# Optimization experiments

Measured on AMD Instinct MI355X. Metric: run time of the kernel, lower is better.

Reference implementation:

```python
import jax, jax.numpy as jnp
import numpy as np

B, IN, HID, EMB, K = 65536, 256, 256, 64, 4096
EPS = 1e-5  # BatchNorm1d default eps


def setup_inputs() -> dict:
    key = jax.random.key(0)
    ks = jax.random.split(key, 12)
    s = 0.05
    return {
        "x": jax.random.normal(ks[0], (B, IN), jnp.float32),
        "W1": jax.random.normal(ks[1], (HID, IN), jnp.float32) * s,
        "b1": jax.random.normal(ks[2], (HID,), jnp.float32) * s,
        "gamma": jnp.ones((HID,), jnp.float32),
        "beta": jnp.zeros((HID,), jnp.float32),
        "mean": jax.random.normal(ks[3], (HID,), jnp.float32) * s,
        "var": jax.random.uniform(ks[4], (HID,), jnp.float32, 0.5, 1.5),
        "W2": jax.random.normal(ks[5], (HID // 2, HID), jnp.float32) * s,
        "b2": jax.random.normal(ks[6], (HID // 2,), jnp.float32) * s,
        "W3": jax.random.normal(ks[7], (EMB, HID // 2), jnp.float32) * s,
        "b3": jax.random.normal(ks[8], (EMB,), jnp.float32) * s,
        "codebook": jax.random.normal(ks[9], (K, EMB), jnp.float32),
    }


def reference(x, W1, b1, gamma, beta, mean, var, W2, b2, W3, b3, codebook):
    # encoder: Linear -> BatchNorm1d (eval stats) -> ReLU -> Linear -> ReLU -> Linear -> Tanh
    h = x @ W1.T + b1                                   # [B, HID]
    h = (h - mean) * jax.lax.rsqrt(var + EPS) * gamma + beta
    h = jax.nn.relu(h)
    h = jax.nn.relu(h @ W2.T + b2)                      # [B, HID//2]
    z = jnp.tanh(h @ W3.T + b3)                         # [B, EMB]
    # squared-distance matrix: ||z||^2 + ||e||^2 - 2 z e^T  -> [B, K]
    d = (jnp.sum(z * z, axis=1, keepdims=True)
         + jnp.sum(codebook * codebook, axis=1)
         - 2.0 * (z @ codebook.T))
    return jnp.argmin(d, axis=1)                        # [B] int token indices
```

## Files before the change

### kernel.cpp

```cpp
#include <hip/hip_runtime.h>

#define IN_DIM  256
#define HID_DIM 256
#define H2_DIM  128
#define EMB_DIM 64
#define K_CODES 4096
#define EPS_BN  1e-5f


typedef _Float16 f16;
typedef _Float16 f16x4 __attribute__((ext_vector_type(4)));
typedef _Float16 f16x8 __attribute__((ext_vector_type(8)));
typedef float    f32x16 __attribute__((ext_vector_type(16)));

__global__ __launch_bounds__(256) void k_norms(const float* __restrict__ cb,
                                               float* __restrict__ norms) {
    int c = blockIdx.x * 256 + threadIdx.x;
    const float4* row = reinterpret_cast<const float4*>(cb + (size_t)c * EMB_DIM);
    float s = 0.f;
#pragma unroll
    for (int i = 0; i < EMB_DIM / 4; ++i) {
        float4 v = row[i];
        s += v.x * v.x + v.y * v.y + v.z * v.z + v.w * v.w;
    }
    norms[c] = 0.5f * s;
}

__global__ __launch_bounds__(256) void k_prep(
    const float* __restrict__ W1, const float* __restrict__ W2,
    const float* __restrict__ W3, const float* __restrict__ cb,
    f16* __restrict__ p1h, f16* __restrict__ p1l,
    f16* __restrict__ p2h, f16* __restrict__ p2l,
    f16* __restrict__ p3h, f16* __restrict__ p3l,
    f16* __restrict__ cfh, f16* __restrict__ cfl) {
    int t = blockIdx.x * 256 + threadIdx.x;
    const float* src; f16 *dh, *dl; int tt, row, k0, K;
    if (t < 8192) {
        tt = t; int f = tt >> 6, l = tt & 63;
        int ct = f & 7, kst = f >> 3;
        row = ct * 32 + (l & 31); k0 = kst * 16 + (l >> 5) * 8;
        src = W1; K = IN_DIM; dh = p1h; dl = p1l;
    } else if (t < 12288) {
        tt = t - 8192; int f = tt >> 6, l = tt & 63;
        int ct = f & 3, kst = f >> 2;
        row = ct * 32 + (l & 31); k0 = kst * 16 + (l >> 5) * 8;
        src = W2; K = HID_DIM; dh = p2h; dl = p2l;
    } else if (t < 13312) {
        tt = t - 12288; int f = tt >> 6, l = tt & 63;
        int ct = f & 1, ks = f >> 1;
        row = ct * 32 + (l & 31); k0 = ks * 16 + (l >> 5) * 8;
        src = W3; K = H2_DIM; dh = p3h; dl = p3l;
    } else {
        tt = t - 13312; int f = tt >> 6, l = tt & 63;
        int ct = f & 3, ks = (f >> 2) & 3, ch = f >> 4;
        row = ch * 128 + ct * 32 + (l & 31); k0 = ks * 16 + (l >> 5) * 8;
        src = cb; K = EMB_DIM; dh = cfh; dl = cfl;
    }
    const float* s = src + (size_t)row * K + k0;
    f16x8 hv, lv;
#pragma unroll
    for (int j = 0; j < 8; ++j) {
        float v = s[j];
        f16 h = (f16)v;
        hv[j] = h;
        lv[j] = (f16)(v - (float)h);
    }
    *(f16x8*)(dh + (size_t)tt * 8) = hv;
    *(f16x8*)(dl + (size_t)tt * 8) = lv;
}

__global__ __launch_bounds__(256) void k_encoder_mfma(
    const float* __restrict__ x,
    const f16* __restrict__ p1h, const f16* __restrict__ p1l,
    const f16* __restrict__ p2h, const f16* __restrict__ p2l,
    const f16* __restrict__ p3h, const f16* __restrict__ p3l,
    const float* __restrict__ b1,
    const float* __restrict__ gm, const float* __restrict__ bt,
    const float* __restrict__ mu, const float* __restrict__ vr,
    const float* __restrict__ b2, const float* __restrict__ b3,
    f16* __restrict__ Zh, f16* __restrict__ Zl) {
    __shared__ __align__(16) f16 sm[25600];
    const int tid  = threadIdx.x;
    const int lane = tid & 63;
    const int w    = tid >> 6;
    const int ln31 = lane & 31;
    const int q    = lane >> 5;
    const int r0   = blockIdx.x * 32;

#pragma unroll
    for (int it = 0; it < 8; ++it) {
        int i = it * 256 + tid;
        int row = i >> 6, c4 = (i & 63) * 4;
        float4 v = *reinterpret_cast<const float4*>(
            x + (size_t)(r0 + row) * IN_DIM + c4);
        f16x4 hv, lv;
        hv[0] = (f16)v.x; lv[0] = (f16)(v.x - (float)hv[0]);
        hv[1] = (f16)v.y; lv[1] = (f16)(v.y - (float)hv[1]);
        hv[2] = (f16)v.z; lv[2] = (f16)(v.z - (float)hv[2]);
        hv[3] = (f16)v.w; lv[3] = (f16)(v.w - (float)hv[3]);
        *(f16x4*)(sm + row * 264 + c4)        = hv;
        *(f16x4*)(sm + 8448 + row * 264 + c4) = lv;
    }
    __syncthreads();

    f32x16 acc1a = {};
    f32x16 acc1b = {};
    {
        const f16* q1h = p1h + (size_t)(2 * w) * 512 + lane * 8;
        const f16* q1l = p1l + (size_t)(2 * w) * 512 + lane * 8;
        f16x8 bh0 = *(const f16x8*)(q1h);
        f16x8 bh1 = *(const f16x8*)(q1h + 512);
        f16x8 bl0 = *(const f16x8*)(q1l);
        f16x8 bl1 = *(const f16x8*)(q1l + 512);
#pragma unroll 2
        for (int kst = 0; kst < 16; ++kst) {
            f16x8 ch0 = bh0, ch1 = bh1, cl0 = bl0, cl1 = bl1;
            int kn = (kst + 1) & 15;
            bh0 = *(const f16x8*)(q1h + (size_t)kn * 4096);
            bh1 = *(const f16x8*)(q1h + (size_t)kn * 4096 + 512);
            bl0 = *(const f16x8*)(q1l + (size_t)kn * 4096);
            bl1 = *(const f16x8*)(q1l + (size_t)kn * 4096 + 512);
            int koff = kst * 16 + q * 8;
            f16x8 ah = *(const f16x8*)(sm + ln31 * 264 + koff);
            f16x8 al = *(const f16x8*)(sm + 8448 + ln31 * 264 + koff);
            acc1a = __builtin_amdgcn_mfma_f32_32x32x16_f16(ah, ch0, acc1a, 0, 0, 0);
            acc1b = __builtin_amdgcn_mfma_f32_32x32x16_f16(ah, ch1, acc1b, 0, 0, 0);
            acc1a = __builtin_amdgcn_mfma_f32_32x32x16_f16(al, ch0, acc1a, 0, 0, 0);
            acc1b = __builtin_amdgcn_mfma_f32_32x32x16_f16(al, ch1, acc1b, 0, 0, 0);
            acc1a = __builtin_amdgcn_mfma_f32_32x32x16_f16(ah, cl0, acc1a, 0, 0, 0);
            acc1b = __builtin_amdgcn_mfma_f32_32x32x16_f16(ah, cl1, acc1b, 0, 0, 0);
        }
    }
    __syncthreads();

    {
#pragma unroll
        for (int nt = 0; nt < 2; ++nt) {
            int j = w * 64 + nt * 32 + ln31;
            float sc = gm[j] * rsqrtf(vr[j] + EPS_BN);
            float sh = (b1[j] - mu[j]) * sc + bt[j];
            const f32x16& a = nt ? acc1b : acc1a;
#pragma unroll
            for (int r = 0; r < 16; ++r) {
                int row = (r & 3) + 8 * (r >> 2) + 4 * q;
                float v = a[r] * sc + sh;
                v = v > 0.f ? v : 0.f;
                f16 h = (f16)v;
                sm[row * 264 + j]        = h;
                sm[8448 + row * 264 + j] = (f16)(v - (float)h);
            }
        }
    }
    __syncthreads();

    f32x16 acc2a = {};
    f32x16 acc2b = {};
    {
        const f16* q2h = p2h + (size_t)w * 512 + lane * 8;
        const f16* q2l = p2l + (size_t)w * 512 + lane * 8;
        f16x8 bh = *(const f16x8*)(q2h);
        f16x8 bl = *(const f16x8*)(q2l);
#pragma unroll 2
        for (int kst = 0; kst < 16; ++kst) {
            f16x8 cbh = bh, cbl = bl;
            int kn = (kst + 1) & 15;
            bh = *(const f16x8*)(q2h + (size_t)kn * 2048);
            bl = *(const f16x8*)(q2l + (size_t)kn * 2048);
            int koff = kst * 16 + q * 8;
            f16x8 ah = *(const f16x8*)(sm + ln31 * 264 + koff);
            f16x8 al = *(const f16x8*)(sm + 8448 + ln31 * 264 + koff);
            f32x16& acc = (kst & 1) ? acc2b : acc2a;
            acc = __builtin_amdgcn_mfma_f32_32x32x16_f16(ah, cbh, acc, 0, 0, 0);
            acc = __builtin_amdgcn_mfma_f32_32x32x16_f16(al, cbh, acc, 0, 0, 0);
            acc = __builtin_amdgcn_mfma_f32_32x32x16_f16(ah, cbl, acc, 0, 0, 0);
        }
    }
    {
        int j2 = w * 32 + ln31;
        float bias = b2[j2];
#pragma unroll
        for (int r = 0; r < 16; ++r) {
            int row = (r & 3) + 8 * (r >> 2) + 4 * q;
            float v = (acc2a[r] + acc2b[r]) + bias;
            v = v > 0.f ? v : 0.f;
            f16 h = (f16)v;
            sm[16896 + row * 136 + j2] = h;
            sm[21248 + row * 136 + j2] = (f16)(v - (float)h);
        }
    }
    __syncthreads();

    if (w < 2) {
        f32x16 acc3a = {};
        f32x16 acc3b = {};
        const f16* q3h = p3h + (size_t)w * 512 + lane * 8;
        const f16* q3l = p3l + (size_t)w * 512 + lane * 8;
        f16x8 bh = *(const f16x8*)(q3h);
        f16x8 bl = *(const f16x8*)(q3l);
#pragma unroll 2
        for (int ks = 0; ks < 8; ++ks) {
            f16x8 cbh = bh, cbl = bl;
            int kn = (ks + 1) & 7;
            bh = *(const f16x8*)(q3h + (size_t)kn * 1024);
            bl = *(const f16x8*)(q3l + (size_t)kn * 1024);
            f16x8 ah = *(const f16x8*)(sm + 16896 + ln31 * 136 + ks * 16 + q * 8);
            f16x8 al = *(const f16x8*)(sm + 21248 + ln31 * 136 + ks * 16 + q * 8);
            f32x16& acc = (ks & 1) ? acc3b : acc3a;
            acc = __builtin_amdgcn_mfma_f32_32x32x16_f16(ah, cbh, acc, 0, 0, 0);
            acc = __builtin_amdgcn_mfma_f32_32x32x16_f16(al, cbh, acc, 0, 0, 0);
            acc = __builtin_amdgcn_mfma_f32_32x32x16_f16(ah, cbl, acc, 0, 0, 0);
        }
        int j3 = w * 32 + ln31;
        float bias = b3[j3];
#pragma unroll
        for (int r = 0; r < 16; ++r) {
            int row = (r & 3) + 8 * (r >> 2) + 4 * q;
            float zv = tanhf((acc3a[r] + acc3b[r]) + bias);
            f16 h = (f16)zv;
            size_t idx = (size_t)(r0 + row) * EMB_DIM + j3;
            Zh[idx] = h;
            Zl[idx] = (f16)(zv - (float)h);
        }
    }
}

__global__ __launch_bounds__(256) void k_argmin_mfma(
    const f16* __restrict__ Zh, const f16* __restrict__ Zl,
    const f16* __restrict__ cfh, const f16* __restrict__ cfl,
    const float* __restrict__ norms, int* __restrict__ out) {
    __shared__ __align__(16) f16 sm[32768];
    const int tid  = threadIdx.x;
    const int lane = tid & 63;
    const int w    = tid >> 6;
    const int ln31 = lane & 31;
    const int q    = lane >> 5;
    const int r0   = blockIdx.x * 128;

    f16x8 ah[4], al[4];
#pragma unroll
    for (int ks = 0; ks < 4; ++ks) {
        size_t zoff = (size_t)(r0 + w * 32 + ln31) * EMB_DIM + ks * 16 + q * 8;
        ah[ks] = *(const f16x8*)(Zh + zoff);
        al[ks] = *(const f16x8*)(Zl + zoff);
    }

    float bv[16];
    int   bi[16];
#pragma unroll
    for (int i = 0; i < 16; ++i) { bv[i] = -3.4e38f; bi[i] = 0; }

#define STAGE(CH, B) do {                                                     \
        const f16* sH_ = cfh + (size_t)(CH) * 8192;                           \
        const f16* sL_ = cfl + (size_t)(CH) * 8192;                           \
        f16* dH_ = sm + (B) * 16384;                                          \
        f16* dL_ = sm + (B) * 16384 + 8192;                                   \
        _Pragma("unroll")                                                     \
        for (int it_ = 0; it_ < 4; ++it_) {                                   \
            int off_ = (it_ * 256 + tid) * 8;                                 \
            __builtin_amdgcn_global_load_lds(                                 \
                (const __attribute__((address_space(1))) void*)(sH_ + off_),  \
                (__attribute__((address_space(3))) void*)(dH_ + off_),        \
                16, 0, 0);                                                    \
            __builtin_amdgcn_global_load_lds(                                 \
                (const __attribute__((address_space(1))) void*)(sL_ + off_),  \
                (__attribute__((address_space(3))) void*)(dL_ + off_),        \
                16, 0, 0);                                                    \
        }                                                                     \
    } while (0)

    STAGE(0, 0);
    __syncthreads();

#pragma unroll 1
    for (int ch = 0; ch < 32; ++ch) {
        int b = ch & 1;
        if (ch + 1 < 32) STAGE(ch + 1, b ^ 1);
        const f16* ebh = sm + b * 16384;
        const f16* ebl = sm + b * 16384 + 8192;
#pragma unroll 2
        for (int ct = 0; ct < 4; ++ct) {
            f16x8 bh[4], bl[4];
#pragma unroll
            for (int ks = 0; ks < 4; ++ks) {
                int off = (ks * 4 + ct) * 512 + lane * 8;
                bh[ks] = *(const f16x8*)(ebh + off);
                bl[ks] = *(const f16x8*)(ebl + off);
            }
            f32x16 acc0 = {};
            f32x16 acc1 = {};
#pragma unroll
            for (int ks = 0; ks < 4; ks += 2) {
                acc0 = __builtin_amdgcn_mfma_f32_32x32x16_f16(ah[ks],     bh[ks],     acc0, 0, 0, 0);
                acc1 = __builtin_amdgcn_mfma_f32_32x32x16_f16(ah[ks + 1], bh[ks + 1], acc1, 0, 0, 0);
                acc0 = __builtin_amdgcn_mfma_f32_32x32x16_f16(al[ks],     bh[ks],     acc0, 0, 0, 0);
                acc1 = __builtin_amdgcn_mfma_f32_32x32x16_f16(al[ks + 1], bh[ks + 1], acc1, 0, 0, 0);
                acc0 = __builtin_amdgcn_mfma_f32_32x32x16_f16(ah[ks],     bl[ks],     acc0, 0, 0, 0);
                acc1 = __builtin_amdgcn_mfma_f32_32x32x16_f16(ah[ks + 1], bl[ks + 1], acc1, 0, 0, 0);
            }
            int   col = ch * 128 + ct * 32 + ln31;
            float nv  = norms[col];
#pragma unroll
            for (int r = 0; r < 16; ++r) {
                float t  = (acc0[r] + acc1[r]) - nv;
                bool  gt = t > bv[r];
                bv[r] = gt ? t : bv[r];
                bi[r] = gt ? col : bi[r];
            }
        }
        __syncthreads();
    }
#undef STAGE

    float* redv = (float*)sm;
    int*   redi = (int*)sm + 4224;
#pragma unroll
    for (int r = 0; r < 16; ++r) {
        int row = w * 32 + (r & 3) + 8 * (r >> 2) + 4 * q;
        redv[row * 33 + ln31] = bv[r];
        redi[row * 33 + ln31] = bi[r];
    }
    __syncthreads();
    if (tid < 128) {
        float v  = redv[tid * 33];
        int   ix = redi[tid * 33];
#pragma unroll
        for (int j = 1; j < 32; ++j) {
            float vj = redv[tid * 33 + j];
            int   ij = redi[tid * 33 + j];
            if (vj > v || (vj == v && ij < ix)) { v = vj; ix = ij; }
        }
        out[r0 + tid] = ix;
    }
}

extern "C" void kernel_launch(void* const* d_in, const int* in_sizes, int n_in,
                              void* d_out, int out_size, void* d_ws, size_t ws_size,
                              hipStream_t stream) {
    (void)n_in; (void)out_size; (void)ws_size;
    const float* x  = (const float*)d_in[0];
    const float* W1 = (const float*)d_in[1];
    const float* b1 = (const float*)d_in[2];
    const float* gm = (const float*)d_in[3];
    const float* bt = (const float*)d_in[4];
    const float* mu = (const float*)d_in[5];
    const float* vr = (const float*)d_in[6];
    const float* W2 = (const float*)d_in[7];
    const float* b2 = (const float*)d_in[8];
    const float* W3 = (const float*)d_in[9];
    const float* b3 = (const float*)d_in[10];
    const float* cb = (const float*)d_in[11];

    char* ws = (char*)d_ws;
    float* norms = (float*)ws;
    f16* cfh = (f16*)(ws + 16384);
    f16* cfl = (f16*)(ws + 540672);
    f16* p1h = (f16*)(ws + 1064960);
    f16* p1l = (f16*)(ws + 1196032);
    f16* p2h = (f16*)(ws + 1327104);
    f16* p2l = (f16*)(ws + 1392640);
    f16* p3h = (f16*)(ws + 1458176);
    f16* p3l = (f16*)(ws + 1474560);
    f16* Zh  = (f16*)(ws + 1490944);
    f16* Zl  = (f16*)(ws + 9879552);
    int* out = (int*)d_out;

    const int B = in_sizes[0] / IN_DIM;

    k_norms<<<K_CODES / 256, 256, 0, stream>>>(cb, norms);
    k_prep<<<180, 256, 0, stream>>>(W1, W2, W3, cb, p1h, p1l, p2h, p2l,
                                    p3h, p3l, cfh, cfl);
    k_encoder_mfma<<<B / 32, 256, 0, stream>>>(x, p1h, p1l, p2h, p2l, p3h, p3l,
                                               b1, gm, bt, mu, vr, b2, b3, Zh, Zl);
    k_argmin_mfma<<<B / 128, 256, 0, stream>>>(Zh, Zl, cfh, cfl, norms, out);
}
```

Measured before the change: 281.6 us.

## Split argmin codebook tiles across two wave groups with 512-thread blocks

The argmin kernel now runs 8 waves per block. Two groups of 4 waves share the same 128 rows but each handles half of the 32-column codebook tiles in every staged chunk. The halves' per-lane best values are merged through LDS before the existing row reduction. This gives more waves per CU to hide LDS and MFMA latency and halves each wave's serial chunk work, at the cost of duplicated Z register loads, an extra LDS merge, and possible register-pressure limits from launch_bounds 512.

```diff
diff --git a/kernel.cpp b/kernel.cpp
--- a/kernel.cpp
+++ b/kernel.cpp
@@ -224,7 +224,7 @@
     }
 }
 
-__global__ __launch_bounds__(256) void k_argmin_mfma(
+__global__ __launch_bounds__(512) void k_argmin_mfma(
     const f16* __restrict__ Zh, const f16* __restrict__ Zl,
     const f16* __restrict__ cfh, const f16* __restrict__ cfl,
     const float* __restrict__ norms, int* __restrict__ out) {
@@ -232,6 +232,8 @@
     const int tid  = threadIdx.x;
     const int lane = tid & 63;
     const int w    = tid >> 6;
+    const int rt   = w & 3;
+    const int hp   = w >> 2;
     const int ln31 = lane & 31;
     const int q    = lane >> 5;
     const int r0   = blockIdx.x * 128;
@@ -239,7 +241,7 @@
     f16x8 ah[4], al[4];
 #pragma unroll
     for (int ks = 0; ks < 4; ++ks) {
-        size_t zoff = (size_t)(r0 + w * 32 + ln31) * EMB_DIM + ks * 16 + q * 8;
+        size_t zoff = (size_t)(r0 + rt * 32 + ln31) * EMB_DIM + ks * 16 + q * 8;
         ah[ks] = *(const f16x8*)(Zh + zoff);
         al[ks] = *(const f16x8*)(Zl + zoff);
     }
@@ -255,8 +257,8 @@
         f16* dH_ = sm + (B) * 16384;                                          \
         f16* dL_ = sm + (B) * 16384 + 8192;                                   \
         _Pragma("unroll")                                                     \
-        for (int it_ = 0; it_ < 4; ++it_) {                                   \
-            int off_ = (it_ * 256 + tid) * 8;                                 \
+        for (int it_ = 0; it_ < 2; ++it_) {                                   \
+            int off_ = (it_ * 512 + tid) * 8;                                 \
             __builtin_amdgcn_global_load_lds(                                 \
                 (const __attribute__((address_space(1))) void*)(sH_ + off_),  \
                 (__attribute__((address_space(3))) void*)(dH_ + off_),        \
@@ -277,8 +279,9 @@
         if (ch + 1 < 32) STAGE(ch + 1, b ^ 1);
         const f16* ebh = sm + b * 16384;
         const f16* ebl = sm + b * 16384 + 8192;
-#pragma unroll 2
-        for (int ct = 0; ct < 4; ++ct) {
+#pragma unroll
+        for (int c2 = 0; c2 < 2; ++c2) {
+            int ct = hp * 2 + c2;
             f16x8 bh[4], bl[4];
 #pragma unroll
             for (int ks = 0; ks < 4; ++ks) {
@@ -311,13 +314,39 @@
     }
 #undef STAGE
 
+    {
+        float* pv = (float*)sm;
+        int*   pi = (int*)sm + 4352;
+        if (hp == 1) {
+#pragma unroll
+            for (int r = 0; r < 16; ++r) {
+                pv[rt * 1088 + lane * 17 + r] = bv[r];
+                pi[rt * 1088 + lane * 17 + r] = bi[r];
+            }
+        }
+        __syncthreads();
+        if (hp == 0) {
+#pragma unroll
+            for (int r = 0; r < 16; ++r) {
+                float v2 = pv[rt * 1088 + lane * 17 + r];
+                int   i2 = pi[rt * 1088 + lane * 17 + r];
+                bool tk = (v2 > bv[r]) || (v2 == bv[r] && i2 < bi[r]);
+                bv[r] = tk ? v2 : bv[r];
+                bi[r] = tk ? i2 : bi[r];
+            }
+        }
+    }
+    __syncthreads();
+
     float* redv = (float*)sm;
     int*   redi = (int*)sm + 4224;
-#pragma unroll
-    for (int r = 0; r < 16; ++r) {
-        int row = w * 32 + (r & 3) + 8 * (r >> 2) + 4 * q;
-        redv[row * 33 + ln31] = bv[r];
-        redi[row * 33 + ln31] = bi[r];
+    if (hp == 0) {
+#pragma unroll
+        for (int r = 0; r < 16; ++r) {
+            int row = rt * 32 + (r & 3) + 8 * (r >> 2) + 4 * q;
+            redv[row * 33 + ln31] = bv[r];
+            redi[row * 33 + ln31] = bi[r];
+        }
     }
     __syncthreads();
     if (tid < 128) {
@@ -371,5 +400,5 @@
                                     p3h, p3l, cfh, cfl);
     k_encoder_mfma<<<B / 32, 256, 0, stream>>>(x, p1h, p1l, p2h, p2l, p3h, p3l,
                                                b1, gm, bt, mu, vr, b2, b3, Zh, Zl);
-    k_argmin_mfma<<<B / 128, 256, 0, stream>>>(Zh, Zl, cfh, cfl, norms, out);
+    k_argmin_mfma<<<B / 128, 512, 0, stream>>>(Zh, Zl, cfh, cfl, norms, out);
 }
```

Result: no change. 277.0 us (-1.6%).
